# Performance work log

Measured on AMD Instinct MI355X. Metric: run time of the kernel, lower is better.

## Reference

```python
import jax, jax.numpy as jnp
import numpy as np

B, S, I, H, O = 8, 2048, 1024, 4096, 1024


def setup_inputs() -> dict:
    key = jax.random.key(0)
    ks = jax.random.split(key, 7)
    s_i = 1.0 / np.sqrt(I)
    s_h = 1.0 / np.sqrt(H)
    return {
        "x": jax.random.normal(ks[0], (B, S, I), dtype=jnp.float32),
        "W1": jax.random.normal(ks[1], (H, I), dtype=jnp.float32) * s_i,
        "b1": jax.random.normal(ks[2], (H,), dtype=jnp.float32) * s_i,
        "W2": jax.random.normal(ks[3], (O, H), dtype=jnp.float32) * s_h,
        "b2": jax.random.normal(ks[4], (O,), dtype=jnp.float32) * s_h,
        "Wg": jax.random.normal(ks[5], (I, I), dtype=jnp.float32) * s_i,
        "bg": jax.random.normal(ks[6], (I,), dtype=jnp.float32) * s_i,
    }


def reference(x, W1, b1, W2, b2, Wg, bg):
    # Gate is a per-timestep linear on x_t only -> batch it over all timesteps.
    decay = jax.nn.sigmoid(jnp.einsum('bsi,ji->bsj', x, Wg) + bg)  # [B,S,I]
    immediate = x * decay
    delayed = (1.0 - decay) * x

    # Sequential buffer recurrence: buf_t = buf_{t-1} * decay_t + delayed_t
    def step(buf, td):
        d, dl = td
        buf = buf * d + dl
        return buf, buf

    buf0 = jnp.zeros((x.shape[0], x.shape[2]), dtype=x.dtype)
    _, bufs = jax.lax.scan(step, buf0, (jnp.swapaxes(decay, 0, 1), jnp.swapaxes(delayed, 0, 1)))  # [S,B,I]
    combined = immediate + jnp.swapaxes(bufs, 0, 1)  # [B,S,I]

    # MLP applied per timestep -> batch over (B,S).
    hidden = jax.nn.relu(jnp.einsum('bsi,hi->bsh', combined, W1) + b1)  # [B,S,H]
    out = jnp.einsum('bsh,oh->bso', hidden, W2) + b2  # [B,S,O]
    return out
```

## Files before the change

### kernel.cpp

```cpp
#include <hip/hip_runtime.h>
#include <hip/hip_bf16.h>
#include <type_traits>

using bf16 = __hip_bfloat16;

typedef __bf16 bf16x8 __attribute__((ext_vector_type(8)));
typedef unsigned short u16x8 __attribute__((ext_vector_type(8)));
typedef float f32x4 __attribute__((ext_vector_type(4)));

constexpr int Bdim = 8, Sdim = 2048, Idim = 1024, Hdim = 4096, Odim = 1024;
constexpr int CH = 64;
constexpr int CL = Sdim / CH;

#define EP_SIGMOID 0
#define EP_RELU    1
#define EP_BIAS    2

__device__ __forceinline__ void async16(void* lds, const void* g) {
    __builtin_amdgcn_global_load_lds(
        (const __attribute__((address_space(1))) unsigned int*)g,
        (__attribute__((address_space(3))) unsigned int*)lds,
        16, 0, 0);
}

__global__ __launch_bounds__(256) void cvt_f32_bf16(const float* __restrict__ in,
                                                    bf16* __restrict__ out, int n) {
    const int i = (blockIdx.x * 256 + threadIdx.x) * 4;
    if (i >= n) return;
    const float4 v = *(const float4*)(in + i);
    union { unsigned short us[4]; unsigned long long u64; } r;
    r.us[0] = __bfloat16_as_ushort(__float2bfloat16(v.x));
    r.us[1] = __bfloat16_as_ushort(__float2bfloat16(v.y));
    r.us[2] = __bfloat16_as_ushort(__float2bfloat16(v.z));
    r.us[3] = __bfloat16_as_ushort(__float2bfloat16(v.w));
    *(unsigned long long*)(out + i) = r.u64;
}

__device__ __forceinline__ u16x8 load8(const float* p) {
    const float4 v0 = *(const float4*)p;
    const float4 v1 = *(const float4*)(p + 4);
    u16x8 r;
    r[0] = __bfloat16_as_ushort(__float2bfloat16(v0.x));
    r[1] = __bfloat16_as_ushort(__float2bfloat16(v0.y));
    r[2] = __bfloat16_as_ushort(__float2bfloat16(v0.z));
    r[3] = __bfloat16_as_ushort(__float2bfloat16(v0.w));
    r[4] = __bfloat16_as_ushort(__float2bfloat16(v1.x));
    r[5] = __bfloat16_as_ushort(__float2bfloat16(v1.y));
    r[6] = __bfloat16_as_ushort(__float2bfloat16(v1.z));
    r[7] = __bfloat16_as_ushort(__float2bfloat16(v1.w));
    return r;
}
__device__ __forceinline__ u16x8 load8(const bf16* p) { return *(const u16x8*)p; }

__device__ __forceinline__ float toF(float v) { return v; }
__device__ __forceinline__ float toF(bf16 v)  { return __bfloat162float(v); }

template <int MODE, int N, int K, typename TA, typename TB, typename TO>
__global__ __launch_bounds__(256) void gemm_bt(const TA* __restrict__ A,
                                               const TB* __restrict__ Bm,
                                               const float* __restrict__ bias,
                                               TO* __restrict__ outp,
                                               int Mt) {
    __shared__ __align__(16) unsigned short Alds[128 * 32];
    __shared__ __align__(16) unsigned short Blds[128 * 32];

    const int tid  = threadIdx.x;
    const int lane = tid & 63;
    const int wave = tid >> 6;
    const int wr = wave >> 1, wc = wave & 1;
    const int quad = lane >> 4, l15 = lane & 15;

    constexpr int Nt = N >> 7;
    constexpr int GRP = 8;
    constexpr int gsz = GRP * Nt;
    const int g   = blockIdx.x / gsz;
    const int rem = blockIdx.x - g * gsz;
    const int mbase = g * GRP;
    int msz = Mt - mbase; if (msz > GRP) msz = GRP;
    const int m_idx = mbase + rem % msz;
    const int n_idx = rem / msz;
    const int m0 = m_idx * 128;
    const int n0 = n_idx * 128;

    const int srow = tid >> 2;
    const int scol = (tid & 3) * 8;
    const TA* ag0 = A  + (size_t)(m0 + srow) * K + scol;
    const TA* ag1 = ag0 + (size_t)64 * K;
    const TB* bg0 = Bm + (size_t)(n0 + srow) * K + scol;
    const TB* bg1 = bg0 + (size_t)64 * K;
    unsigned short* al0 = Alds + tid * 8;
    unsigned short* al1 = al0 + 2048;
    unsigned short* bl0 = Blds + tid * 8;
    unsigned short* bl1 = bl0 + 2048;

    f32x4 acc[4][4];
#pragma unroll
    for (int i = 0; i < 4; ++i)
#pragma unroll
        for (int j = 0; j < 4; ++j) acc[i][j] = {0.f, 0.f, 0.f, 0.f};

    constexpr bool FAST = std::is_same_v<TA, bf16> && std::is_same_v<TB, bf16>;

#pragma unroll 8
    for (int k0 = 0; k0 < K; k0 += 32) {
        if constexpr (FAST) {
            async16(al0, ag0); async16(al1, ag1);
            async16(bl0, bg0); async16(bl1, bg1);
        } else {
            const u16x8 a0 = load8(ag0), a1 = load8(ag1);
            const u16x8 b0 = load8(bg0), b1 = load8(bg1);
            *(u16x8*)al0 = a0; *(u16x8*)al1 = a1;
            *(u16x8*)bl0 = b0; *(u16x8*)bl1 = b1;
        }
        ag0 += 32; ag1 += 32; bg0 += 32; bg1 += 32;
        __syncthreads();

        bf16x8 af[4], bfv[4];
#pragma unroll
        for (int mi = 0; mi < 4; ++mi) {
            const u16x8 t = *(const u16x8*)(Alds + (wr * 64 + mi * 16 + l15) * 32 + quad * 8);
            af[mi] = __builtin_bit_cast(bf16x8, t);
        }
#pragma unroll
        for (int ni = 0; ni < 4; ++ni) {
            const u16x8 t = *(const u16x8*)(Blds + (wc * 64 + ni * 16 + l15) * 32 + quad * 8);
            bfv[ni] = __builtin_bit_cast(bf16x8, t);
        }
#pragma unroll
        for (int mi = 0; mi < 4; ++mi)
#pragma unroll
            for (int ni = 0; ni < 4; ++ni)
                acc[mi][ni] = __builtin_amdgcn_mfma_f32_16x16x32_bf16(af[mi], bfv[ni], acc[mi][ni], 0, 0, 0);
        __syncthreads();
    }

#pragma unroll
    for (int ni = 0; ni < 4; ++ni) {
        const int ncol = n0 + wc * 64 + ni * 16 + l15;
        const float bv = bias[ncol];
#pragma unroll
        for (int mi = 0; mi < 4; ++mi) {
            const int mrow = m0 + wr * 64 + mi * 16 + quad * 4;
#pragma unroll
            for (int r = 0; r < 4; ++r) {
                float v = acc[mi][ni][r] + bv;
                if constexpr (MODE == EP_SIGMOID) v = 1.f / (1.f + __expf(-v));
                if constexpr (MODE == EP_RELU)    v = v > 0.f ? v : 0.f;
                if constexpr (std::is_same_v<TO, bf16>)
                    outp[(size_t)(mrow + r) * N + ncol] = __float2bfloat16(v);
                else
                    outp[(size_t)(mrow + r) * N + ncol] = v;
            }
        }
    }
}

template <typename XT>
__global__ __launch_bounds__(256) void scan_p1(const XT* __restrict__ x,
                                               const bf16* __restrict__ decay,
                                               float* __restrict__ P,
                                               float* __restrict__ Q) {
    const int tid = threadIdx.x;
    const int blk = blockIdx.x;
    const int itile = blk & 3;
    const int bc = blk >> 2;
    const int c = bc & (CH - 1);
    const int b = bc >> 6;
    const int i = itile * 256 + tid;
    size_t idx = ((size_t)(b * Sdim + c * CL)) * Idim + i;
    float p = 1.f, q = 0.f;
#pragma unroll 4
    for (int j = 0; j < CL; ++j) {
        const float d = __bfloat162float(decay[idx]);
        const float xx = toF(x[idx]);
        q = q * d + (1.f - d) * xx;
        p *= d;
        idx += Idim;
    }
    P[(size_t)bc * Idim + i] = p;
    Q[(size_t)bc * Idim + i] = q;
}

__global__ __launch_bounds__(256) void scan_p2(const float* __restrict__ P,
                                               const float* __restrict__ Q,
                                               float* __restrict__ buf0,
                                               int G) {
    const int g = blockIdx.x * 256 + threadIdx.x;
    const int b = g >> 10;
    const int i = g & (Idim - 1);
    if (b >= G) return;
    float buf = 0.f;
    for (int c = 0; c < CH; ++c) {
        const size_t o = ((size_t)(b * CH + c)) * Idim + i;
        buf0[o] = buf;
        buf = P[o] * buf + Q[o];
    }
}

template <typename XT>
__global__ __launch_bounds__(256) void scan_p3(const XT* __restrict__ x,
                                               const bf16* __restrict__ decay,
                                               const float* __restrict__ buf0,
                                               bf16* __restrict__ comb) {
    const int tid = threadIdx.x;
    const int blk = blockIdx.x;
    const int itile = blk & 3;
    const int bc = blk >> 2;
    const int c = bc & (CH - 1);
    const int b = bc >> 6;
    const int i = itile * 256 + tid;
    size_t idx = ((size_t)(b * Sdim + c * CL)) * Idim + i;
    float buf = buf0[(size_t)bc * Idim + i];
#pragma unroll 4
    for (int j = 0; j < CL; ++j) {
        const float d = __bfloat162float(decay[idx]);
        const float xx = toF(x[idx]);
        buf = buf * d + (1.f - d) * xx;
        comb[idx] = __float2bfloat16(xx * d + buf);
        idx += Idim;
    }
}

extern "C" void kernel_launch(void* const* d_in, const int* in_sizes, int n_in,
                              void* d_out, int out_size, void* d_ws, size_t ws_size,
                              hipStream_t stream) {
    const float* x  = (const float*)d_in[0];
    const float* W1 = (const float*)d_in[1];
    const float* b1 = (const float*)d_in[2];
    const float* W2 = (const float*)d_in[3];
    const float* b2 = (const float*)d_in[4];
    const float* Wg = (const float*)d_in[5];
    const float* bg = (const float*)d_in[6];
    float* out = (float*)d_out;

    const dim3 blk(256);

    const size_t nW1 = (size_t)Hdim * Idim;
    const size_t nW2 = (size_t)Odim * Hdim;
    const size_t nWg = (size_t)Idim * Idim;
    const size_t wCopies = (nW1 + nW2 + nWg) * 2;

    const size_t xbB   = (size_t)Sdim * Idim * 2;
    const size_t dB    = xbB;
    const size_t cmbB  = xbB;
    const size_t pB    = (size_t)CH * Idim * 4;
    const size_t perBatch = xbB + dB + cmbB + 3 * pB;

    int G = 0;
    if (ws_size >= wCopies + 8 * perBatch) G = 8;
    else if (ws_size >= wCopies + 4 * perBatch) G = 4;
    else if (ws_size >= wCopies + 2 * perBatch) G = 2;
    else if (ws_size >= wCopies + 1 * perBatch) G = 1;

    if (G > 0) {
        char* p = (char*)d_ws;
        bf16* W1b = (bf16*)p;  p += nW1 * 2;
        bf16* W2b = (bf16*)p;  p += nW2 * 2;
        bf16* Wgb = (bf16*)p;  p += nWg * 2;
        bf16*  xb   = (bf16*)p;
        bf16*  decay= (bf16*)(p + (size_t)G * xbB);
        bf16*  comb = (bf16*)(p + (size_t)G * (xbB + dB));
        float* P    = (float*)(p + (size_t)G * (xbB + dB + cmbB));
        float* Q    = (float*)(p + (size_t)G * (xbB + dB + cmbB + pB));
        float* buf0 = (float*)(p + (size_t)G * (xbB + dB + cmbB + 2 * pB));
        bf16*  hid  = xb;
        const int chunk_rows = G * 1024;

        cvt_f32_bf16<<<(int)(nW1 / 1024), blk, 0, stream>>>(W1, W1b, (int)nW1);
        cvt_f32_bf16<<<(int)(nW2 / 1024), blk, 0, stream>>>(W2, W2b, (int)nW2);
        cvt_f32_bf16<<<(int)(nWg / 1024), blk, 0, stream>>>(Wg, Wgb, (int)nWg);

        for (int b0 = 0; b0 < Bdim; b0 += G) {
            const float* xg = x + (size_t)b0 * Sdim * Idim;
            const int rowsG = G * Sdim;
            const int nXg = rowsG * Idim;

            cvt_f32_bf16<<<nXg / 1024, blk, 0, stream>>>(xg, xb, nXg);

            gemm_bt<EP_SIGMOID, Idim, Idim, bf16, bf16, bf16>
                <<<(Idim / 128) * (rowsG / 128), blk, 0, stream>>>(
                    xb, Wgb, bg, decay, rowsG / 128);

            scan_p1<bf16><<<G * CH * (Idim / 256), blk, 0, stream>>>(xb, decay, P, Q);
            scan_p2<<<G * Idim / 256, blk, 0, stream>>>(P, Q, buf0, G);
            scan_p3<bf16><<<G * CH * (Idim / 256), blk, 0, stream>>>(xb, decay, buf0, comb);

            for (int r0 = 0; r0 < rowsG; r0 += chunk_rows) {
                const int rows = (rowsG - r0 < chunk_rows) ? rowsG - r0 : chunk_rows;
                gemm_bt<EP_RELU, Hdim, Idim, bf16, bf16, bf16>
                    <<<(Hdim / 128) * (rows / 128), blk, 0, stream>>>(
                        comb + (size_t)r0 * Idim, W1b, b1, hid, rows / 128);
                gemm_bt<EP_BIAS, Odim, Hdim, bf16, bf16, float>
                    <<<(Odim / 128) * (rows / 128), blk, 0, stream>>>(
                        hid, W2b, b2, out + (size_t)(b0 * Sdim + r0) * Odim, rows / 128);
            }
        }
    } else {
        char* p = (char*)d_ws;
        bf16*  decay= (bf16*)p;
        bf16*  comb = (bf16*)(p + dB);
        float* P    = (float*)(p + dB + cmbB);
        float* Q    = (float*)(p + dB + cmbB + pB);
        float* buf0 = (float*)(p + dB + cmbB + 2 * pB);
        char*  hp   = p + dB + cmbB + 3 * pB;
        size_t rem  = (ws_size > (size_t)(hp - (char*)d_ws))
                        ? ws_size - (size_t)(hp - (char*)d_ws) : 0;
        int chunk_rows = (int)((rem / ((size_t)Hdim * 2)) / 128) * 128;
        if (chunk_rows < 128) chunk_rows = 128;
        if (chunk_rows > Sdim) chunk_rows = Sdim;
        bf16* hid = (bf16*)hp;

        for (int b0 = 0; b0 < Bdim; ++b0) {
            const float* xg = x + (size_t)b0 * Sdim * Idim;

            gemm_bt<EP_SIGMOID, Idim, Idim, float, float, bf16>
                <<<(Idim / 128) * (Sdim / 128), blk, 0, stream>>>(
                    xg, Wg, bg, decay, Sdim / 128);

            scan_p1<float><<<CH * (Idim / 256), blk, 0, stream>>>(xg, decay, P, Q);
            scan_p2<<<Idim / 256, blk, 0, stream>>>(P, Q, buf0, 1);
            scan_p3<float><<<CH * (Idim / 256), blk, 0, stream>>>(xg, decay, buf0, comb);

            for (int r0 = 0; r0 < Sdim; r0 += chunk_rows) {
                const int rows = (Sdim - r0 < chunk_rows) ? Sdim - r0 : chunk_rows;
                gemm_bt<EP_RELU, Hdim, Idim, bf16, float, bf16>
                    <<<(Hdim / 128) * (rows / 128), blk, 0, stream>>>(
                        comb + (size_t)r0 * Idim, W1, b1, hid, rows / 128);
                gemm_bt<EP_BIAS, Odim, Hdim, bf16, float, float>
                    <<<(Odim / 128) * (rows / 128), blk, 0, stream>>>(
                        hid, W2, b2, out + (size_t)(b0 * Sdim + r0) * Odim, rows / 128);
            }
        }
    }
}
```

Before: 565.1 us.

## Add 8-wave 256x256-tile pipelined GEMM with swizzled LDS and XCD-aware block mapping

Introduces a new GEMM kernel with 512 threads and 256-wide (or 128) by 256 tiles. It double-buffers LDS with async global-to-LDS loads that are staged in halves and interleaved with MFMA quarters between barriers. It also adds an XOR-swizzled LDS layout, s_setprio around MFMA bursts, and a block remap that groups work per XCD. All three GEMMs (gate, W1, W2) in the main path switch to it, aiming for more data reuse per tile and overlap of memory loads with compute. The price is more LDS per block, fewer blocks on small problems, and fragile hand-written waitcnt ordering.

```diff
diff --git a/kernel.cpp b/kernel.cpp
--- a/kernel.cpp
+++ b/kernel.cpp
@@ -141,6 +141,186 @@
 #pragma unroll
         for (int mi = 0; mi < 4; ++mi) {
             const int mrow = m0 + wr * 64 + mi * 16 + quad * 4;
+#pragma unroll
+            for (int r = 0; r < 4; ++r) {
+                float v = acc[mi][ni][r] + bv;
+                if constexpr (MODE == EP_SIGMOID) v = 1.f / (1.f + __expf(-v));
+                if constexpr (MODE == EP_RELU)    v = v > 0.f ? v : 0.f;
+                if constexpr (std::is_same_v<TO, bf16>)
+                    outp[(size_t)(mrow + r) * N + ncol] = __float2bfloat16(v);
+                else
+                    outp[(size_t)(mrow + r) * N + ncol] = v;
+            }
+        }
+    }
+}
+
+template <int MODE, int BM, int N, int K, typename TO>
+__global__ __launch_bounds__(512, 2) void gemm8p(const bf16* __restrict__ A,
+                                                 const bf16* __restrict__ Bm,
+                                                 const float* __restrict__ bias,
+                                                 TO* __restrict__ outp,
+                                                 int Mt) {
+    static_assert(BM == 256 || BM == 128);
+    constexpr int MR   = BM / 32;
+    constexpr int MR2  = MR / 2;
+    constexpr int ABUF = BM * 128;
+    constexpr int BBUF = 256 * 128;
+    constexpr int HALF_A = ABUF / 2;
+    constexpr int HALF_B = BBUF / 2;
+    constexpr int LA = BM / 128;
+    constexpr int NT = K / 64;
+    static_assert(NT % 2 == 0 && NT >= 2);
+
+    __shared__ __align__(16) char lds[2 * ABUF + 2 * BBUF];
+
+    const int tid  = threadIdx.x;
+    const int lane = tid & 63;
+    const int wave = tid >> 6;
+    const int wr = wave >> 2;
+    const int wc = wave & 3;
+    const int quad = lane >> 4, l15 = lane & 15;
+
+    constexpr int Nt = N / 256;
+    const int nwg = Mt * Nt;
+    int b = blockIdx.x;
+    if ((nwg & 7) == 0) { const int cpx = nwg >> 3; b = (b & 7) * cpx + (b >> 3); }
+    const int m_idx = b % Mt;
+    const int n_idx = b / Mt;
+    const int m0 = m_idx * BM;
+    const int n0 = n_idx * 256;
+
+    const int loff = (l15 * 64 + quad * 16) ^ ((l15 >> 3) << 5);
+
+    char* const Ab0 = lds;
+    char* const Ab1 = lds + ABUF;
+    char* const Bb0 = lds + 2 * ABUF;
+    char* const Bb1 = lds + 2 * ABUF + BBUF;
+
+    int rowS[2], klS[2];
+#pragma unroll
+    for (int l = 0; l < 2; ++l) {
+        const int s = l * 512 + tid;
+        const int c = s & 63;
+        const int e = c ^ (((c >> 5) & 1) << 1);
+        rowS[l] = ((s >> 7) << 4) + (e >> 2);
+        klS[l]  = ((s >> 6) & 1) * 32 + (e & 3) * 8;
+    }
+    const bf16* pa[2]; const bf16* pb[2];
+#pragma unroll
+    for (int l = 0; l < 2; ++l) {
+        pa[l] = A  + (size_t)(m0 + rowS[l]) * K + klS[l];
+        pb[l] = Bm + (size_t)(n0 + rowS[l]) * K + klS[l];
+    }
+
+    auto stageA = [&](char* dst, int h, int kt) {
+#pragma unroll
+        for (int l = 0; l < LA; ++l)
+            async16(dst + h * HALF_A + (l * 512 + tid) * 16,
+                    pa[l] + (size_t)h * (BM / 2) * K + (size_t)kt * 64);
+    };
+    auto stageB = [&](char* dst, int h, int kt) {
+#pragma unroll
+        for (int l = 0; l < 2; ++l)
+            async16(dst + h * HALF_B + (l * 512 + tid) * 16,
+                    pb[l] + (size_t)h * 128 * K + (size_t)kt * 64);
+    };
+    auto ldA = [&](const char* abase, int mi_g, int ks) -> bf16x8 {
+        return __builtin_bit_cast(bf16x8,
+            *(const u16x8*)(abase + (((wr * MR + mi_g) * 2 + ks) << 10) + loff));
+    };
+    auto ldB = [&](const char* bbase, int ni, int ks) -> bf16x8 {
+        return __builtin_bit_cast(bf16x8,
+            *(const u16x8*)(bbase + (((wc * 4 + ni) * 2 + ks) << 10) + loff));
+    };
+
+    f32x4 acc[MR][4];
+#pragma unroll
+    for (int i = 0; i < MR; ++i)
+#pragma unroll
+        for (int j = 0; j < 4; ++j) acc[i][j] = {0.f, 0.f, 0.f, 0.f};
+    bf16x8 a[MR2][2], bb[4][2];
+
+    stageA(Ab0, 0, 0); stageA(Ab0, 1, 0);
+    stageB(Bb0, 0, 0); stageB(Bb0, 1, 0);
+    stageB(Bb1, 0, 1); stageB(Bb1, 1, 1);
+    asm volatile("s_waitcnt vmcnt(4)" ::: "memory");
+    __builtin_amdgcn_s_barrier();
+
+#define FENCE() asm volatile("" ::: "memory")
+#define MFMA_Q(AR, NI0)                                                         \
+    _Pragma("unroll") for (int mi = 0; mi < MR2; ++mi)                          \
+    _Pragma("unroll") for (int ni = 0; ni < 2; ++ni)                            \
+    _Pragma("unroll") for (int ks = 0; ks < 2; ++ks)                            \
+        acc[(AR) + mi][(NI0) + ni] = __builtin_amdgcn_mfma_f32_16x16x32_bf16(   \
+            a[mi][ks], bb[(NI0) + ni][ks], acc[(AR) + mi][(NI0) + ni], 0, 0, 0);
+
+#define KTILE(T, AB, BB, AN)                                                    \
+    {                                                                           \
+        const int t_ = (T);                                                     \
+                                   \
+        _Pragma("unroll") for (int mi = 0; mi < MR2; ++mi)                      \
+        _Pragma("unroll") for (int ks = 0; ks < 2; ++ks)                        \
+            a[mi][ks] = ldA(AB, mi, ks);                                        \
+        _Pragma("unroll") for (int ni = 0; ni < 2; ++ni)                        \
+        _Pragma("unroll") for (int ks = 0; ks < 2; ++ks)                        \
+            bb[ni][ks] = ldB(BB, ni, ks);                                       \
+        if (t_ + 1 < NT) stageA(AN, 0, t_ + 1);                                 \
+        FENCE(); __builtin_amdgcn_s_barrier();                                  \
+        asm volatile("s_waitcnt lgkmcnt(0)" ::: "memory");                      \
+        __builtin_amdgcn_s_setprio(1);                                          \
+        MFMA_Q(0, 0)                                                            \
+        __builtin_amdgcn_s_setprio(0);                                          \
+        FENCE(); __builtin_amdgcn_s_barrier();                                  \
+                                          \
+        _Pragma("unroll") for (int ni = 0; ni < 2; ++ni)                        \
+        _Pragma("unroll") for (int ks = 0; ks < 2; ++ks)                        \
+            bb[2 + ni][ks] = ldB(BB, 2 + ni, ks);                               \
+        if (t_ + 1 < NT) stageA(AN, 1, t_ + 1);                                 \
+        FENCE(); __builtin_amdgcn_s_barrier();                                  \
+        asm volatile("s_waitcnt lgkmcnt(0)" ::: "memory");                      \
+        __builtin_amdgcn_s_setprio(1);                                          \
+        MFMA_Q(0, 2)                                                            \
+        __builtin_amdgcn_s_setprio(0);                                          \
+        FENCE(); __builtin_amdgcn_s_barrier();                                  \
+          \
+        _Pragma("unroll") for (int mi = 0; mi < MR2; ++mi)                      \
+        _Pragma("unroll") for (int ks = 0; ks < 2; ++ks)                        \
+            a[mi][ks] = ldA(AB, MR2 + mi, ks);                                  \
+        if (t_ + 2 < NT) stageB(BB, 0, t_ + 2);                                 \
+        FENCE(); __builtin_amdgcn_s_barrier();                                  \
+        asm volatile("s_waitcnt lgkmcnt(0)" ::: "memory");                      \
+        __builtin_amdgcn_s_setprio(1);                                          \
+        MFMA_Q(MR2, 0)                                                          \
+        __builtin_amdgcn_s_setprio(0);                                          \
+        FENCE(); __builtin_amdgcn_s_barrier();                                  \
+                          \
+        if (t_ + 2 < NT) stageB(BB, 1, t_ + 2);                                 \
+        FENCE(); __builtin_amdgcn_s_barrier();                                  \
+        __builtin_amdgcn_s_setprio(1);                                          \
+        MFMA_Q(MR2, 2)                                                          \
+        __builtin_amdgcn_s_setprio(0);                                          \
+        if (t_ + 2 < NT) { asm volatile("s_waitcnt vmcnt(4)" ::: "memory"); }   \
+        else             { asm volatile("s_waitcnt vmcnt(0)" ::: "memory"); }   \
+        FENCE(); __builtin_amdgcn_s_barrier();                                  \
+    }
+
+#pragma unroll 1
+    for (int t = 0; t < NT; t += 2) {
+        KTILE(t,     Ab0, Bb0, Ab1)
+        KTILE(t + 1, Ab1, Bb1, Ab0)
+    }
+#undef KTILE
+#undef MFMA_Q
+#undef FENCE
+
+#pragma unroll
+    for (int ni = 0; ni < 4; ++ni) {
+        const int ncol = n0 + wc * 64 + ni * 16 + l15;
+        const float bv = bias[ncol];
+#pragma unroll
+        for (int mi = 0; mi < MR; ++mi) {
+            const int mrow = m0 + wr * (MR * 16) + mi * 16 + quad * 4;
 #pragma unroll
             for (int r = 0; r < 4; ++r) {
                 float v = acc[mi][ni][r] + bv;
@@ -234,6 +414,7 @@
     float* out = (float*)d_out;
 
     const dim3 blk(256);
+    const dim3 blk512(512);
 
     const size_t nW1 = (size_t)Hdim * Idim;
     const size_t nW2 = (size_t)Odim * Hdim;
@@ -277,9 +458,9 @@
 
             cvt_f32_bf16<<<nXg / 1024, blk, 0, stream>>>(xg, xb, nXg);
 
-            gemm_bt<EP_SIGMOID, Idim, Idim, bf16, bf16, bf16>
-                <<<(Idim / 128) * (rowsG / 128), blk, 0, stream>>>(
-                    xb, Wgb, bg, decay, rowsG / 128);
+            gemm8p<EP_SIGMOID, 256, Idim, Idim, bf16>
+                <<<(rowsG / 256) * (Idim / 256), blk512, 0, stream>>>(
+                    xb, Wgb, bg, decay, rowsG / 256);
 
             scan_p1<bf16><<<G * CH * (Idim / 256), blk, 0, stream>>>(xb, decay, P, Q);
             scan_p2<<<G * Idim / 256, blk, 0, stream>>>(P, Q, buf0, G);
@@ -287,11 +468,11 @@
 
             for (int r0 = 0; r0 < rowsG; r0 += chunk_rows) {
                 const int rows = (rowsG - r0 < chunk_rows) ? rowsG - r0 : chunk_rows;
-                gemm_bt<EP_RELU, Hdim, Idim, bf16, bf16, bf16>
-                    <<<(Hdim / 128) * (rows / 128), blk, 0, stream>>>(
-                        comb + (size_t)r0 * Idim, W1b, b1, hid, rows / 128);
-                gemm_bt<EP_BIAS, Odim, Hdim, bf16, bf16, float>
-                    <<<(Odim / 128) * (rows / 128), blk, 0, stream>>>(
+                gemm8p<EP_RELU, 256, Hdim, Idim, bf16>
+                    <<<(rows / 256) * (Hdim / 256), blk512, 0, stream>>>(
+                        comb + (size_t)r0 * Idim, W1b, b1, hid, rows / 256);
+                gemm8p<EP_BIAS, 128, Odim, Hdim, float>
+                    <<<(rows / 128) * (Odim / 256), blk512, 0, stream>>>(
                         hid, W2b, b2, out + (size_t)(b0 * Sdim + r0) * Odim, rows / 128);
             }
         }
```

New measurement: 519.1 us. -8.1%, faster.
